# Kernel tuning notes

Measured on AMD Instinct MI355X. Metric: run time of the kernel, lower is better.

The kernel has to match this reference:

```python
import jax, jax.numpy as jnp
import numpy as np

DIM = 1024; HEADS = 8; DHEAD = 64; INNER = HEADS * DHEAD
WS = 512; B = 2; N = 2048; FF = 4 * DIM
NEG = -1e9


def layernorm(x, g, b, eps=1e-5):
    mu = jnp.mean(x, -1, keepdims=True)
    var = jnp.mean((x - mu) ** 2, -1, keepdims=True)
    return (x - mu) * jax.lax.rsqrt(var + eps) * g + b


def rmsnorm(x, g, eps=1e-6):
    return x * jax.lax.rsqrt(jnp.mean(x * x, -1, keepdims=True) + eps) * g


def rotate_half(x):
    x1, x2 = jnp.split(x, 2, -1)
    return jnp.concatenate([-x2, x1], -1)


def local_attention(q, k, v):
    # lucidrains LocalAttention: single-head over last dim, rotary pos emb,
    # window_size=WS, causal, look_backward=1, look_forward=0. n % WS == 0 so autopad no-op.
    b, n, d = q.shape
    w = n // WS
    inv_freq = 1.0 / (10000.0 ** (jnp.arange(0, d, 2, dtype=jnp.float32) / d))
    t = jnp.arange(n)
    freqs = t[:, None].astype(jnp.float32) * inv_freq[None, :]
    emb = jnp.concatenate([freqs, freqs], -1)           # [n, d]
    cos, sin = jnp.cos(emb), jnp.sin(emb)
    q = q * cos + rotate_half(q) * sin
    k = k * cos + rotate_half(k) * sin
    bq = q.reshape(b, w, WS, d) * (d ** -0.5)
    bk = k.reshape(b, w, WS, d)
    bv = v.reshape(b, w, WS, d)

    def look_around(x, pad_value):
        # gather current window + 1 window backward along the window axis
        pads = [(0, 0), (1, 0)] + [(0, 0)] * (x.ndim - 2)
        xp = jnp.pad(x, pads, constant_values=pad_value)
        return jnp.concatenate([xp[:, 0:w], xp[:, 1:w + 1]], axis=2)

    bk = look_around(bk, 0.0)                 # [b, w, 2*WS, d]
    bv = look_around(bv, 0.0)
    bt = t.reshape(w, WS)                     # query positions per window
    bqk = look_around(bt[None], -1)[0]        # key positions, pad = -1  [w, 2*WS]
    sim = jnp.einsum('bwie,bwje->bwij', bq, bk)  # [b, w, WS, 2*WS]
    mask = (bt[:, :, None] < bqk[:, None, :]) | (bqk[:, None, :] == -1)
    sim = jnp.where(mask[None], NEG, sim)
    attn = jax.nn.softmax(sim, -1)
    out = jnp.einsum('bwij,bwje->bwie', attn, bv)
    return out.reshape(b, n, d)


def setup_inputs() -> dict:
    key = jax.random.key(0)
    ks = jax.random.split(key, 10)
    s = 0.02
    f32 = jnp.float32
    return {
        'text': jax.random.normal(ks[0], (B, N, DIM), f32),
        'audio': jax.random.normal(ks[1], (B, N, DIM), f32),
        'video': jax.random.normal(ks[2], (B, N, DIM), f32),
        'Wa': jax.random.normal(ks[3], (DIM, DIM), f32) * s,
        'ba': jnp.zeros((DIM,), f32),
        'lna_g': jnp.ones((DIM,), f32), 'lna_b': jnp.zeros((DIM,), f32),
        'Wvid': jax.random.normal(ks[4], (DIM, DIM), f32) * s,
        'bvid': jnp.zeros((DIM,), f32),
        'lnv_g': jnp.ones((DIM,), f32), 'lnv_b': jnp.zeros((DIM,), f32),
        'ln1_g': jnp.ones((DIM,), f32), 'ln1_b': jnp.zeros((DIM,), f32),
        'Wq': jax.random.normal(ks[5], (DIM, INNER), f32) * s,
        'Wkv': jax.random.normal(ks[6], (DIM, 2 * INNER), f32) * s,
        'qn_g': jnp.ones((DHEAD,), f32), 'kn_g': jnp.ones((DHEAD,), f32),
        'Wo': jax.random.normal(ks[7], (INNER, DIM), f32) * s,
        'W1': jax.random.normal(ks[8], (DIM, FF), f32) * s,
        'b1': jnp.zeros((FF,), f32),
        'ln2_g': jnp.ones((FF,), f32), 'ln2_b': jnp.zeros((FF,), f32),
        'W2': jax.random.normal(ks[9], (FF, DIM), f32) * s,
        'b2': jnp.zeros((DIM,), f32),
    }


def reference(text, audio, video, Wa, ba, lna_g, lna_b, Wvid, bvid, lnv_g, lnv_b,
              ln1_g, ln1_b, Wq, Wkv, qn_g, kn_g, Wo, W1, b1, ln2_g, ln2_b, W2, b2):
    # modality -> text-token adapters (audio_to_text / video_to_text): linear + layernorm
    audio_t = layernorm(audio @ Wa + ba, lna_g, lna_b)
    video_t = layernorm(video @ Wvid + bvid, lnv_g, lnv_b)
    # windowed local attention: q=text, k=audio tokens, v=video tokens
    x = local_attention(text, audio_t, video_t)          # [B, N, DIM]
    # qk-norm full causal attention (flash=False: dense [B,H,N,N] scores)
    b, n, _ = x.shape
    h = layernorm(x, ln1_g, ln1_b)
    q = (h @ Wq).reshape(b, n, HEADS, DHEAD).transpose(0, 2, 1, 3)
    k, v = jnp.split(h @ Wkv, 2, -1)
    k = k.reshape(b, n, HEADS, DHEAD).transpose(0, 2, 1, 3)
    v = v.reshape(b, n, HEADS, DHEAD).transpose(0, 2, 1, 3)
    q = rmsnorm(q, qn_g)
    k = rmsnorm(k, kn_g)
    sim = jnp.einsum('bhid,bhjd->bhij', q, k) * (DHEAD ** -0.5)
    causal = jnp.tril(jnp.ones((n, n), bool))
    sim = jnp.where(causal[None, None], sim, NEG)
    attn = jax.nn.softmax(sim, -1)
    o = jnp.einsum('bhij,bhjd->bhid', attn, v).transpose(0, 2, 1, 3).reshape(b, n, INNER)
    x = o @ Wo
    x = x + x                                            # x = x + x in source
    # FFN: Linear -> GELU -> post-act LayerNorm -> Linear, + residual
    h1 = layernorm(jax.nn.gelu(x @ W1 + b1), ln2_g, ln2_b)
    return h1 @ W2 + b2 + x
```

## Files before the change

kernel.cpp:

```cpp
#include <hip/hip_runtime.h>
#include <hip/hip_bf16.h>

typedef __bf16 bf16;
typedef __bf16 bf16x8 __attribute__((ext_vector_type(8)));
typedef float  f32x4  __attribute__((ext_vector_type(4)));

static __device__ __forceinline__ float b2f(bf16 x) { return (float)x; }
static __device__ __forceinline__ bf16  f2b(float x) { return (bf16)x; }
static __device__ __forceinline__ float ldval(float v) { return v; }
static __device__ __forceinline__ float ldval(bf16 v)  { return (float)v; }

static __device__ __forceinline__ void gl_lds16(const bf16* g, bf16* l)
{
    __builtin_amdgcn_global_load_lds(
        (const __attribute__((address_space(1))) void*)g,
        (__attribute__((address_space(3))) void*)l,
        16, 0, 0);
}

__global__ void detect_dtype(const unsigned short* __restrict__ p, int* __restrict__ flag)
{
    if (threadIdx.x == 0 && blockIdx.x == 0) {
        int big = 0;
        for (int i = 0; i < 512; ++i) {
            int e = (p[i] >> 7) & 0xFF;
            if (e >= 0xE0) big++;
        }
        *flag = (big > 0) ? 1 : 0;
    }
}

__global__ __launch_bounds__(256) void convert2(
    const void* __restrict__ sa, const void* __restrict__ sb,
    bf16* __restrict__ da, bf16* __restrict__ db, int n,
    const int* __restrict__ flag)
{
    int f = *flag;
    int half = gridDim.x >> 1;
    const void* s = (blockIdx.x < half) ? sa : sb;
    bf16* d = (blockIdx.x < half) ? da : db;
    int bid = (blockIdx.x < half) ? blockIdx.x : blockIdx.x - half;
    for (int i = bid * 256 + threadIdx.x; i < n; i += half * 256) {
        float v = f ? ((const float*)s)[i] : (float)((const bf16*)s)[i];
        d[i] = f2b(v);
    }
}

struct VecPack { const void* src[14]; int n[14]; };
__global__ __launch_bounds__(256) void convert_vecs(
    VecPack vp, bf16* __restrict__ dst, const int* __restrict__ flag)
{
    int v = blockIdx.x;
    int f = *flag;
    const void* s = vp.src[v];
    int n = vp.n[v];
    bf16* d = dst + (size_t)v * 4096;
    for (int i = threadIdx.x; i < n; i += 256) {
        float x = f ? ((const float*)s)[i] : (float)((const bf16*)s)[i];
        d[i] = f2b(x);
    }
}

template <int EPI, int MT>
__global__ __launch_bounds__(256) void gemm_bt(
    const bf16* __restrict__ A0, int lda, int zsA, int zsA2,
    const bf16* __restrict__ B0, int ldb, int zsB, int zsB2,
    void* __restrict__ C0, int ldc, int zsC, int zsC2,
    const bf16* __restrict__ bias, int zsBias, float scale, int K)
{
    constexpr int IFR = MT / 32;
    __shared__ __align__(16) bf16 As[MT * 64];
    __shared__ __align__(16) bf16 Bs[128 * 64];
    const int z = blockIdx.z;
    const bf16* A  = A0 + (size_t)z * zsA + (size_t)(z >> 2) * zsA2;
    const bf16* Bt = B0 + (size_t)z * zsB + (size_t)(z >> 2) * zsB2;
    const size_t cbase = (size_t)z * zsC + (size_t)(z >> 2) * zsC2;
    if (bias) bias += (size_t)z * zsBias;
    const int tid  = threadIdx.x;
    const int lane = tid & 63, wave = tid >> 6;
    const int quad = lane >> 4, l16 = lane & 15;
    const size_t tm = (size_t)blockIdx.y * MT, tn = (size_t)blockIdx.x * 128;
    const int wm = (wave >> 1) * (MT / 2), wn = (wave & 1) * 64;
    const int srow = lane >> 3;
    const int scol = ((lane & 7) ^ srow) * 8;

    f32x4 acc[IFR][4];
    const f32x4 zro = {0.f, 0.f, 0.f, 0.f};
    #pragma unroll
    for (int i = 0; i < IFR; ++i)
        #pragma unroll
        for (int j = 0; j < 4; ++j) acc[i][j] = zro;

    const int swzA = l16 & 7;
    for (int k0 = 0; k0 < K; k0 += 64) {
        #pragma unroll
        for (int i = 0; i < IFR; ++i) {
            int chunk = (wave * IFR + i) * 64;
            int row = (chunk >> 3) + srow;
            gl_lds16(A + (tm + row) * (size_t)lda + k0 + scol, As + (size_t)chunk * 8);
        }
        #pragma unroll
        for (int i = 0; i < 4; ++i) {
            int chunk = (wave * 4 + i) * 64;
            int row = (chunk >> 3) + srow;
            gl_lds16(Bt + (tn + row) * (size_t)ldb + k0 + scol, Bs + (size_t)chunk * 8);
        }
        __syncthreads();
        #pragma unroll
        for (int kk = 0; kk < 2; ++kk) {
            bf16x8 af[IFR], bfr[4];
            #pragma unroll
            for (int i = 0; i < IFR; ++i) {
                int row = wm + i * 16 + l16;
                af[i] = *(const bf16x8*)(const void*)&As[(row * 8 + ((kk*4 + quad) ^ swzA)) * 8];
            }
            #pragma unroll
            for (int j = 0; j < 4; ++j) {
                int row = wn + j * 16 + l16;
                bfr[j] = *(const bf16x8*)(const void*)&Bs[(row * 8 + ((kk*4 + quad) ^ swzA)) * 8];
            }
            #pragma unroll
            for (int i = 0; i < IFR; ++i)
                #pragma unroll
                for (int j = 0; j < 4; ++j)
                    acc[i][j] = __builtin_amdgcn_mfma_f32_16x16x32_bf16(
                        af[i], bfr[j], acc[i][j], 0, 0, 0);
        }
        __syncthreads();
    }

    float* Cf = (float*)C0;
    bf16*  Cb = (bf16*)C0;
    #pragma unroll
    for (int i = 0; i < IFR; ++i) {
        #pragma unroll
        for (int j = 0; j < 4; ++j) {
            size_t col = tn + wn + j*16 + l16;
            float bb = bias ? b2f(bias[col]) : 0.f;
            #pragma unroll
            for (int r = 0; r < 4; ++r) {
                size_t row = tm + wm + i*16 + quad*4 + r;
                float v = acc[i][j][r] + bb;
                size_t off = cbase + row * (size_t)ldc + col;
                if (EPI == 0) {
                    Cf[off] = v;
                } else if (EPI == 1) {
                    Cb[off] = f2b(v * scale);
                } else {
                    float g = 0.5f * v * (1.f + tanhf(0.7978845608028654f *
                                  (v + 0.044715f * v * v * v)));
                    Cb[off] = f2b(g);
                }
            }
        }
    }
}

__global__ __launch_bounds__(512, 2) void gemm_ff1_8ph(
    const bf16* __restrict__ A, int lda,
    const bf16* __restrict__ Bt, int ldb,
    bf16* __restrict__ C, int ldc,
    const bf16* __restrict__ bias, int K)
{
    __shared__ __align__(16) bf16 As[2][256 * 64];
    __shared__ __align__(16) bf16 Bs[2][256 * 64];
    const int tid  = threadIdx.x;
    const int lane = tid & 63, wave = tid >> 6;
    const int quad = lane >> 4, l16 = lane & 15;
    const int wr = wave >> 2, wc = wave & 3;
    const size_t tm = (size_t)blockIdx.y * 256;
    const size_t tn = (size_t)blockIdx.x * 256;
    const int srow = lane >> 3;
    const int scol = ((lane & 7) ^ srow) * 8;
    const int swz  = l16 & 7;

    f32x4 acc[8][4];
    const f32x4 zro = {0.f, 0.f, 0.f, 0.f};
    #pragma unroll
    for (int m = 0; m < 8; ++m)
        #pragma unroll
        for (int n = 0; n < 4; ++n) acc[m][n] = zro;

    const bf16* aSrc[4];
    const bf16* bSrc[4];
    #pragma unroll
    for (int i = 0; i < 4; ++i) {
        int grow = wave * 32 + i * 8 + srow;
        aSrc[i] = A  + (tm + grow) * (size_t)lda + scol;
        bSrc[i] = Bt + (tn + grow) * (size_t)ldb + scol;
    }

#define STAGE(BUF, K0, I)                                                     \
    do {                                                                      \
        gl_lds16(aSrc[I] + (K0), &As[BUF][(wave * 4 + (I)) * 512]);           \
        gl_lds16(bSrc[I] + (K0), &Bs[BUF][(wave * 4 + (I)) * 512]);           \
    } while (0)

#define LDA_F(BUF, M, KK)                                                     \
    (*(const bf16x8*)(const void*)&As[BUF][(wr * 128 + (M) * 16 + l16) * 64 + \
        ((((KK) * 4 + quad) ^ swz) << 3)])
#define LDB_F(BUF, N, KK)                                                     \
    (*(const bf16x8*)(const void*)&Bs[BUF][(wc * 64 + (N) * 16 + l16) * 64 +  \
        ((((KK) * 4 + quad) ^ swz) << 3)])

#define PHASE(M0, M1, PREF_STMT, TAIL_STMT)                                   \
    {                                                                         \
        PREF_STMT;                                                            \
        bf16x8 x0 = LDA_F(cur, M0, 0), x1 = LDA_F(cur, M0, 1);                \
        bf16x8 y0 = LDA_F(cur, M1, 0), y1 = LDA_F(cur, M1, 1);                \
        asm volatile("s_barrier" ::: "memory");                               \
        __builtin_amdgcn_s_setprio(1);                                        \
        _Pragma("unroll")                                                     \
        for (int n = 0; n < 4; ++n) {                                         \
            acc[M0][n] = __builtin_amdgcn_mfma_f32_16x16x32_bf16(x0, bfr[n][0], acc[M0][n], 0, 0, 0); \
            acc[M0][n] = __builtin_amdgcn_mfma_f32_16x16x32_bf16(x1, bfr[n][1], acc[M0][n], 0, 0, 0); \
            acc[M1][n] = __builtin_amdgcn_mfma_f32_16x16x32_bf16(y0, bfr[n][0], acc[M1][n], 0, 0, 0); \
            acc[M1][n] = __builtin_amdgcn_mfma_f32_16x16x32_bf16(y1, bfr[n][1], acc[M1][n], 0, 0, 0); \
        }                                                                     \
        __builtin_amdgcn_s_setprio(0);                                        \
        TAIL_STMT;                                                            \
        asm volatile("s_barrier" ::: "memory");                               \
    }

    #pragma unroll
    for (int i = 0; i < 4; ++i) STAGE(0, 0, i);
    asm volatile("s_waitcnt vmcnt(0)" ::: "memory");
    asm volatile("s_barrier" ::: "memory");

    const int NT = K >> 6;
    bf16x8 bfr[4][2];
    for (int t = 0; t < NT; ++t) {
        const int cur = t & 1, nxt = cur ^ 1;
        const int k1  = (t + 1) << 6;
        const bool pref = (t + 1 < NT);

        #pragma unroll
        for (int n = 0; n < 4; ++n) {
            bfr[n][0] = LDB_F(cur, n, 0);
            bfr[n][1] = LDB_F(cur, n, 1);
        }
        PHASE(0, 1,
              if (pref) { STAGE(nxt, k1, 0); STAGE(nxt, k1, 1); }, )
        PHASE(2, 3,
              if (pref) { STAGE(nxt, k1, 2); STAGE(nxt, k1, 3); }, )
        PHASE(4, 5, , )
        PHASE(6, 7, ,
              asm volatile("s_waitcnt vmcnt(0)" ::: "memory"))
    }
#undef PHASE
#undef LDB_F
#undef LDA_F
#undef STAGE

    #pragma unroll
    for (int m = 0; m < 8; ++m) {
        #pragma unroll
        for (int n = 0; n < 4; ++n) {
            size_t col = tn + wc * 64 + n * 16 + l16;
            float bb = b2f(bias[col]);
            #pragma unroll
            for (int r = 0; r < 4; ++r) {
                size_t row = tm + wr * 128 + m * 16 + quad * 4 + r;
                float v = acc[m][n][r] + bb;
                float s = v * (1.5957691216057308f + 0.07135481627f * v * v);
                float g = v / (1.f + __expf(-s));
                C[row * (size_t)ldc + col] = f2b(g);
            }
        }
    }
}

__global__ void transpose_any(const void* __restrict__ in, int R, int C,
                              unsigned short* __restrict__ out, int ldo,
                              const int* __restrict__ flag)
{
    __shared__ unsigned short t[32][33];
    int f = *flag;
    int c0 = blockIdx.x * 32, r0 = blockIdx.y * 32;
    int tx = threadIdx.x, ty = threadIdx.y;
    for (int i = ty; i < 32; i += 8) {
        size_t idx = (size_t)(r0 + i) * C + c0 + tx;
        bf16 v = f ? f2b(((const float*)in)[idx]) : ((const bf16*)in)[idx];
        t[i][tx] = *(unsigned short*)&v;
    }
    __syncthreads();
    for (int i = ty; i < 32; i += 8)
        out[(size_t)(c0 + i) * ldo + r0 + tx] = t[tx][i];
}

__global__ void transpose_vt(const unsigned short* __restrict__ in,
                             unsigned short* __restrict__ out)
{
    __shared__ unsigned short t[32][33];
    int b = blockIdx.z;
    const unsigned short* src = in + (size_t)b * 2048 * 1024;
    unsigned short* dst = out + (size_t)b * 1024 * 2560;
    int c0 = blockIdx.x * 32, r0 = blockIdx.y * 32;
    int tx = threadIdx.x, ty = threadIdx.y;
    for (int i = ty; i < 32; i += 8)
        t[i][tx] = src[(size_t)(r0 + i) * 1024 + c0 + tx];
    __syncthreads();
    for (int i = ty; i < 32; i += 8)
        dst[(size_t)(c0 + i) * 2560 + 512 + r0 + tx] = t[tx][i];
}

__global__ void transpose_v(const float* __restrict__ qkv, bf16* __restrict__ Vt)
{
    __shared__ float t[32][33];
    int bh = blockIdx.z, b = bh >> 3, h = bh & 7;
    const float* src = qkv + (size_t)b * 2048 * 1536 + 1024 + h * 64;
    int c0 = blockIdx.x * 32, r0 = blockIdx.y * 32;
    int tx = threadIdx.x, ty = threadIdx.y;
    for (int i = ty; i < 32; i += 8)
        t[i][tx] = src[(size_t)(r0 + i) * 1536 + c0 + tx];
    __syncthreads();
    bf16* dst = Vt + (size_t)bh * 64 * 2048;
    for (int i = ty; i < 32; i += 8)
        dst[(size_t)(c0 + i) * 2048 + r0 + tx] = f2b(t[tx][i]);
}

template <typename Tin>
__global__ __launch_bounds__(256) void ln_rows(
    const Tin* __restrict__ in, int C,
    const bf16* __restrict__ g, const bf16* __restrict__ b,
    bf16* __restrict__ out, float eps)
{
    const int row = blockIdx.x, tid = threadIdx.x;
    const Tin* p = in + (size_t)row * C;
    float s = 0.f, ss = 0.f;
    for (int c = tid; c < C; c += 256) {
        float v = ldval(p[c]);
        s += v; ss += v * v;
    }
    #pragma unroll
    for (int d = 32; d > 0; d >>= 1) { s += __shfl_xor(s, d); ss += __shfl_xor(ss, d); }
    __shared__ float red[2][4];
    int wave = tid >> 6, lane = tid & 63;
    if (lane == 0) { red[0][wave] = s; red[1][wave] = ss; }
    __syncthreads();
    s  = red[0][0] + red[0][1] + red[0][2] + red[0][3];
    ss = red[1][0] + red[1][1] + red[1][2] + red[1][3];
    float mu   = s / C;
    float var  = ss / C - mu * mu;
    float rstd = rsqrtf(var + eps);
    bf16* q = out + (size_t)row * C;
    for (int c = tid; c < C; c += 256) {
        float v = ldval(p[c]);
        q[c] = f2b((v - mu) * rstd * b2f(g[c]) + b2f(b[c]));
    }
}

__global__ __launch_bounds__(256) void ln_rows2(
    const bf16* __restrict__ in,
    const bf16* __restrict__ g0, const bf16* __restrict__ b0,
    const bf16* __restrict__ g1, const bf16* __restrict__ b1,
    bf16* __restrict__ out0, bf16* __restrict__ out1)
{
    const int row = blockIdx.x, tid = threadIdx.x;
    const int sel = row >> 12;
    const bf16* p = in + (size_t)row * 1024;
    const bf16* g = sel ? g1 : g0;
    const bf16* b = sel ? b1 : b0;
    bf16* q = (sel ? out1 + (size_t)(row - 4096) * 1024 : out0 + (size_t)row * 1024);
    float s = 0.f, ss = 0.f;
    for (int c = tid; c < 1024; c += 256) {
        float v = b2f(p[c]);
        s += v; ss += v * v;
    }
    #pragma unroll
    for (int d = 32; d > 0; d >>= 1) { s += __shfl_xor(s, d); ss += __shfl_xor(ss, d); }
    __shared__ float red[2][4];
    int wave = tid >> 6, lane = tid & 63;
    if (lane == 0) { red[0][wave] = s; red[1][wave] = ss; }
    __syncthreads();
    s  = red[0][0] + red[0][1] + red[0][2] + red[0][3];
    ss = red[1][0] + red[1][1] + red[1][2] + red[1][3];
    float mu   = s * (1.f / 1024.f);
    float var  = ss * (1.f / 1024.f) - mu * mu;
    float rstd = rsqrtf(var + 1e-5f);
    for (int c = tid; c < 1024; c += 256) {
        float v = b2f(p[c]);
        q[c] = f2b((v - mu) * rstd * b2f(g[c]) + b2f(b[c]));
    }
}

__global__ __launch_bounds__(256) void rotary_kernel(
    const void* __restrict__ text, const int* __restrict__ flag,
    const bf16* __restrict__ audioT,
    bf16* __restrict__ qrot, bf16* __restrict__ krotPad)
{
    int row = blockIdx.x;
    int t = row & 2047, b = row >> 11;
    int tid = threadIdx.x;
    int f = *flag;
    const float lg = 9.210340371976184f / 512.f;
    size_t base = (size_t)row * 1024;
    size_t kb = ((size_t)(b * 2560 + 512 + t)) * 1024;
    for (int c = tid; c < 512; c += 256) {
        float invf = __expf(-(float)c * lg);
        float th = (float)t * invf;
        float sn, cs;
        sincosf(th, &sn, &cs);
        float q1 = f ? ((const float*)text)[base + c]
                     : b2f(((const bf16*)text)[base + c]);
        float q2 = f ? ((const float*)text)[base + c + 512]
                     : b2f(((const bf16*)text)[base + c + 512]);
        qrot[base + c]       = f2b((q1 * cs - q2 * sn) * 0.03125f);
        qrot[base + c + 512] = f2b((q2 * cs + q1 * sn) * 0.03125f);
        float k1 = b2f(audioT[base + c]), k2 = b2f(audioT[base + c + 512]);
        krotPad[kb + c]       = f2b(k1 * cs - k2 * sn);
        krotPad[kb + c + 512] = f2b(k2 * cs + k1 * sn);
    }
}

__global__ __launch_bounds__(256) void softmax_local(
    const float* __restrict__ sim, bf16* __restrict__ attn)
{
    int i  = blockIdx.x;
    int zz = blockIdx.y;
    int w  = zz & 3;
    int tid = threadIdx.x;
    const float* p = sim + ((size_t)zz * 512 + i) * 1024;
    bf16* q = attn + ((size_t)zz * 512 + i) * 1024;
    int jlo = (w == 0) ? 512 : 0;
    int jhi = 512 + i;
    float m = -1e30f;
    #pragma unroll
    for (int k = 0; k < 4; ++k) {
        int c = tid + k * 256;
        if (c >= jlo && c <= jhi) m = fmaxf(m, p[c]);
    }
    #pragma unroll
    for (int d = 32; d > 0; d >>= 1) m = fmaxf(m, __shfl_xor(m, d));
    __shared__ float red[2][4];
    int wave = tid >> 6, lane = tid & 63;
    if (lane == 0) red[0][wave] = m;
    __syncthreads();
    m = fmaxf(fmaxf(red[0][0], red[0][1]), fmaxf(red[0][2], red[0][3]));
    float pv[4];
    float s = 0.f;
    #pragma unroll
    for (int k = 0; k < 4; ++k) {
        int c = tid + k * 256;
        float e = (c >= jlo && c <= jhi) ? __expf(p[c] - m) : 0.f;
        pv[k] = e; s += e;
    }
    #pragma unroll
    for (int d = 32; d > 0; d >>= 1) s += __shfl_xor(s, d);
    if (lane == 0) red[1][wave] = s;
    __syncthreads();
    s = red[1][0] + red[1][1] + red[1][2] + red[1][3];
    float inv = 1.f / s;
    #pragma unroll
    for (int k = 0; k < 4; ++k) q[tid + k * 256] = f2b(pv[k] * inv);
}

__global__ __launch_bounds__(256) void pack_qk(
    const float* __restrict__ qkv, bf16* __restrict__ Qp, bf16* __restrict__ Kp,
    const bf16* __restrict__ qn_g, const bf16* __restrict__ kn_g)
{
    int gid  = blockIdx.x * 4 + (threadIdx.x >> 6);
    int lane = threadIdx.x & 63;
    int token = gid >> 4, r = gid & 15, part = r >> 3, h = r & 7;
    const float* p = qkv + (size_t)token * 1536 + part * 512 + h * 64 + lane;
    float v = *p;
    float ss = v * v;
    #pragma unroll
    for (int d = 32; d > 0; d >>= 1) ss += __shfl_xor(ss, d);
    float sc = rsqrtf(ss * (1.f / 64.f) + 1e-6f);
    const bf16* gw = part ? kn_g : qn_g;
    float outv = v * sc * b2f(gw[lane]);
    if (!part) outv *= 0.125f;
    int b = token >> 11, t = token & 2047;
    bf16* dst = (part ? Kp : Qp) + ((size_t)(b * 8 + h) * 2048 + t) * 64 + lane;
    *dst = f2b(outv);
}

__global__ __launch_bounds__(256) void flash_fused(
    const bf16* __restrict__ Qp, const bf16* __restrict__ Kp,
    const bf16* __restrict__ Vt, bf16* __restrict__ o)
{
    __shared__ __align__(16) bf16 Ks[2][64][72];
    __shared__ __align__(16) bf16 Vs[2][64][72];
    __shared__ __align__(16) bf16 Ps[4][16][72];
    const int qb = 31 - blockIdx.x;
    const int bh = blockIdx.y, b = bh >> 3, h = bh & 7;
    const int qm = qb * 64;
    const int tid = threadIdx.x, wave = tid >> 6, lane = tid & 63;
    const int quad = lane >> 4, l16 = lane & 15;
    const bf16* Qg = Qp + (size_t)bh * 2048 * 64;
    const bf16* Kg = Kp + (size_t)bh * 2048 * 64;
    const bf16* Vg = Vt + (size_t)bh * 64 * 2048;

    const int qrow = qm + wave * 16 + l16;
    bf16x8 qa[2];
    qa[0] = *(const bf16x8*)(const void*)(Qg + (size_t)qrow * 64 + quad * 8);
    qa[1] = *(const bf16x8*)(const void*)(Qg + (size_t)qrow * 64 + 32 + quad * 8);

    f32x4 oacc[4];
    const f32x4 zro = {0.f, 0.f, 0.f, 0.f};
    #pragma unroll
    for (int j = 0; j < 4; ++j) oacc[j] = zro;
    float mst[4] = {-1e30f, -1e30f, -1e30f, -1e30f};
    float lst[4] = {0.f, 0.f, 0.f, 0.f};

    const int ldr = tid >> 2, ldc = (tid & 3) * 16;
    {
        uint4 ka = *(const uint4*)(const void*)(Kg + (size_t)ldr * 64 + ldc);
        uint4 kb = *(const uint4*)(const void*)(Kg + (size_t)ldr * 64 + ldc + 8);
        uint4 va = *(const uint4*)(const void*)(Vg + (size_t)ldr * 2048 + ldc);
        uint4 vb = *(const uint4*)(const void*)(Vg + (size_t)ldr * 2048 + ldc + 8);
        *(uint4*)(void*)&Ks[0][ldr][ldc]     = ka;
        *(uint4*)(void*)&Ks[0][ldr][ldc + 8] = kb;
        *(uint4*)(void*)&Vs[0][ldr][ldc]     = va;
        *(uint4*)(void*)&Vs[0][ldr][ldc + 8] = vb;
    }
    __syncthreads();

    const int ntiles = qb + 1;
    for (int t = 0; t < ntiles; ++t) {
        const int cur = t & 1, nxt = cur ^ 1;
        const int jt = t * 64;
        const bool pref = (t + 1 < ntiles);
        uint4 ka, kb, va, vb;
        if (pref) {
            int jn = jt + 64;
            ka = *(const uint4*)(const void*)(Kg + (size_t)(jn + ldr) * 64 + ldc);
            kb = *(const uint4*)(const void*)(Kg + (size_t)(jn + ldr) * 64 + ldc + 8);
            va = *(const uint4*)(const void*)(Vg + (size_t)ldr * 2048 + jn + ldc);
            vb = *(const uint4*)(const void*)(Vg + (size_t)ldr * 2048 + jn + ldc + 8);
        }

        f32x4 s[4];
        #pragma unroll
        for (int j = 0; j < 4; ++j) s[j] = zro;
        #pragma unroll
        for (int kk = 0; kk < 2; ++kk) {
            #pragma unroll
            for (int j = 0; j < 4; ++j) {
                bf16x8 kf = *(const bf16x8*)(const void*)&Ks[cur][j*16 + l16][kk*32 + quad*8];
                s[j] = __builtin_amdgcn_mfma_f32_16x16x32_bf16(qa[kk], kf, s[j], 0, 0, 0);
            }
        }

        if (jt + 63 > qm + wave * 16) {
            #pragma unroll
            for (int j = 0; j < 4; ++j) {
                int key = jt + j * 16 + l16;
                #pragma unroll
                for (int r = 0; r < 4; ++r) {
                    int row = qm + wave * 16 + quad * 4 + r;
                    if (key > row) s[j][r] = -1e30f;
                }
            }
        }

        f32x4 tmax = s[0];
        #pragma unroll
        for (int j = 1; j < 4; ++j)
            #pragma unroll
            for (int r = 0; r < 4; ++r) tmax[r] = fmaxf(tmax[r], s[j][r]);
        #pragma unroll
        for (int r = 0; r < 4; ++r) {
            float tv = tmax[r];
            #pragma unroll
            for (int d = 1; d < 16; d <<= 1) tv = fmaxf(tv, __shfl_xor(tv, d));
            tmax[r] = tv;
        }
        float scl[4];
        #pragma unroll
        for (int r = 0; r < 4; ++r) {
            float mn = fmaxf(mst[r], tmax[r]);
            scl[r] = __expf(mst[r] - mn);
            mst[r] = mn;
        }
        f32x4 psum = zro;
        #pragma unroll
        for (int j = 0; j < 4; ++j)
            #pragma unroll
            for (int r = 0; r < 4; ++r) {
                float e = __expf(s[j][r] - mst[r]);
                s[j][r] = e;
                psum[r] += e;
            }
        #pragma unroll
        for (int r = 0; r < 4; ++r) {
            float tv = psum[r];
            #pragma unroll
            for (int d = 1; d < 16; d <<= 1) tv += __shfl_xor(tv, d);
            lst[r] = lst[r] * scl[r] + tv;
        }
        #pragma unroll
        for (int j = 0; j < 4; ++j)
            #pragma unroll
            for (int r = 0; r < 4; ++r) oacc[j][r] *= scl[r];

        #pragma unroll
        for (int j = 0; j < 4; ++j)
            #pragma unroll
            for (int r = 0; r < 4; ++r)
                Ps[wave][quad*4 + r][j*16 + l16] = f2b(s[j][r]);
        bf16x8 pa[2];
        pa[0] = *(const bf16x8*)(const void*)&Ps[wave][l16][quad*8];
        pa[1] = *(const bf16x8*)(const void*)&Ps[wave][l16][32 + quad*8];

        #pragma unroll
        for (int kk = 0; kk < 2; ++kk) {
            #pragma unroll
            for (int j = 0; j < 4; ++j) {
                bf16x8 vf = *(const bf16x8*)(const void*)&Vs[cur][j*16 + l16][kk*32 + quad*8];
                oacc[j] = __builtin_amdgcn_mfma_f32_16x16x32_bf16(pa[kk], vf, oacc[j], 0, 0, 0);
            }
        }

        if (pref) {
            *(uint4*)(void*)&Ks[nxt][ldr][ldc]     = ka;
            *(uint4*)(void*)&Ks[nxt][ldr][ldc + 8] = kb;
            *(uint4*)(void*)&Vs[nxt][ldr][ldc]     = va;
            *(uint4*)(void*)&Vs[nxt][ldr][ldc + 8] = vb;
            __syncthreads();
        }
    }

    #pragma unroll
    for (int j = 0; j < 4; ++j) {
        #pragma unroll
        for (int r = 0; r < 4; ++r) {
            int t = qm + wave * 16 + quad * 4 + r;
            o[((size_t)(b * 2048 + t)) * 512 + h * 64 + j * 16 + l16] =
                f2b(oacc[j][r] / lst[r]);
        }
    }
}

__global__ __launch_bounds__(256) void combine_ff2(
    const float* __restrict__ p0, const float* __restrict__ p1,
    const bf16* __restrict__ x2, const bf16* __restrict__ b2,
    float* __restrict__ out)
{
    int i4 = (blockIdx.x * 256 + threadIdx.x) * 4;
    #pragma unroll
    for (int k = 0; k < 4; ++k) {
        int i = i4 + k;
        out[i] = p0[i] + p1[i] + b2f(x2[i]) + b2f(b2[i & 1023]);
    }
}

static void launch_gemm(int epi, hipStream_t s,
                        const bf16* A, int lda, int zsA, int zsA2,
                        const bf16* Bt, int ldb, int zsB, int zsB2,
                        void* C, int ldc, int zsC, int zsC2,
                        const bf16* bias, int zsBias, float scale,
                        int M, int N, int K, int nz)
{
    bool mt64 = ((M >> 7) * (N >> 7) * nz) <= 512;
    dim3 blk(256);
    if (mt64) {
        dim3 g(N / 128, M / 64, nz);
        switch (epi) {
        case 0: gemm_bt<0,64><<<g, blk, 0, s>>>(A, lda, zsA, zsA2, Bt, ldb, zsB, zsB2, C, ldc, zsC, zsC2, bias, zsBias, scale, K); break;
        case 1: gemm_bt<1,64><<<g, blk, 0, s>>>(A, lda, zsA, zsA2, Bt, ldb, zsB, zsB2, C, ldc, zsC, zsC2, bias, zsBias, scale, K); break;
        default: gemm_bt<2,64><<<g, blk, 0, s>>>(A, lda, zsA, zsA2, Bt, ldb, zsB, zsB2, C, ldc, zsC, zsC2, bias, zsBias, scale, K); break;
        }
    } else {
        dim3 g(N / 128, M / 128, nz);
        switch (epi) {
        case 0: gemm_bt<0,128><<<g, blk, 0, s>>>(A, lda, zsA, zsA2, Bt, ldb, zsB, zsB2, C, ldc, zsC, zsC2, bias, zsBias, scale, K); break;
        case 1: gemm_bt<1,128><<<g, blk, 0, s>>>(A, lda, zsA, zsA2, Bt, ldb, zsB, zsB2, C, ldc, zsC, zsC2, bias, zsBias, scale, K); break;
        default: gemm_bt<2,128><<<g, blk, 0, s>>>(A, lda, zsA, zsA2, Bt, ldb, zsB, zsB2, C, ldc, zsC, zsC2, bias, zsBias, scale, K); break;
        }
    }
}

extern "C" void kernel_launch(void* const* d_in, const int* in_sizes, int n_in,
                              void* d_out, int out_size, void* d_ws, size_t ws_size,
                              hipStream_t stream)
{
    const void* text  = d_in[0];
    const void* audio = d_in[1];
    const void* video = d_in[2];
    const void* Wa    = d_in[3];
    const void* ba    = d_in[4];
    const void* lna_g = d_in[5];
    const void* lna_b = d_in[6];
    const void* Wvid  = d_in[7];
    const void* bvid  = d_in[8];
    const void* lnv_g = d_in[9];
    const void* lnv_b = d_in[10];
    const void* ln1_g = d_in[11];
    const void* ln1_b = d_in[12];
    const void* Wq    = d_in[13];
    const void* Wkv   = d_in[14];
    const void* qn_g  = d_in[15];
    const void* kn_g  = d_in[16];
    const void* Wo    = d_in[17];
    const void* W1    = d_in[18];
    const void* b1    = d_in[19];
    const void* ln2_g = d_in[20];
    const void* ln2_b = d_in[21];
    const void* W2    = d_in[22];
    const void* b2    = d_in[23];

    char* ws = (char*)d_ws;
    size_t off = 0;
    auto alloc = [&](size_t bytes) -> char* {
        char* p = ws + off;
        off += (bytes + 255) & ~(size_t)255;
        return p;
    };
    const size_t MB = 1024 * 1024;
    int*  flag  = (int*)alloc(256);
    bf16* vecs  = (bf16*)alloc(14 * 4096 * 2);
    bf16* WqkvT = (bf16*)alloc((size_t)1536 * 1024 * 2);
    bf16* WoT   = (bf16*)alloc((size_t)1024 * 512 * 2);
    bf16* W1T   = (bf16*)alloc((size_t)4096 * 1024 * 2);
    bf16* W2T   = (bf16*)alloc((size_t)1024 * 4096 * 2);
    char* regionIn = alloc(24 * MB);
    char* region2  = alloc(32 * MB);
    char* regionH  = alloc(8 * MB);
    char* regionX  = alloc(8 * MB);
    char* regionO  = alloc(4 * MB);
    bf16* qrot    = (bf16*)alloc((size_t)4096 * 1024 * 2);
    bf16* krotPad = (bf16*)alloc((size_t)2 * 2560 * 1024 * 2);
    bf16* VTpad   = (bf16*)alloc((size_t)2 * 1024 * 2560 * 2);
    bf16* attn    = (bf16*)alloc((size_t)8 * 512 * 1024 * 2);

    bf16*  audioC = (bf16*)regionIn;
    bf16*  videoC = audioC + (size_t)4096 * 1024;
    float* qkvF   = (float*)regionIn;
    bf16*  tmp2   = (bf16*)region2;
    float* tmpF   = (float*)region2;
    float* xF     = (float*)(region2 + 16 * MB);
    bf16*  g      = (bf16*)region2;
    bf16*  audioT = (bf16*)regionH;
    bf16*  h      = (bf16*)regionH;
    bf16*  videoT = (bf16*)regionX;
    bf16*  x2     = (bf16*)regionX;
    bf16*  WaT    = (bf16*)regionO;
    bf16*  WvT    = WaT + (size_t)1024 * 1024;
    bf16*  o      = (bf16*)regionO;
    bf16*  Qp     = qrot;
    bf16*  Kp     = krotPad;
    bf16*  Vth    = attn;
    float* p0     = (float*)regionIn;
    float* p1     = (float*)VTpad;

    bf16* baC   = vecs + 0 * 4096;
    bf16* bvidC = vecs + 1 * 4096;
    bf16* lnagC = vecs + 2 * 4096;
    bf16* lnabC = vecs + 3 * 4096;
    bf16* lnvgC = vecs + 4 * 4096;
    bf16* lnvbC = vecs + 5 * 4096;
    bf16* ln1gC = vecs + 6 * 4096;
    bf16* ln1bC = vecs + 7 * 4096;
    bf16* qngC  = vecs + 8 * 4096;
    bf16* kngC  = vecs + 9 * 4096;
    bf16* b1C   = vecs + 10 * 4096;
    bf16* ln2gC = vecs + 11 * 4096;
    bf16* ln2bC = vecs + 12 * 4096;
    bf16* b2C   = vecs + 13 * 4096;

    detect_dtype<<<1, 64, 0, stream>>>((const unsigned short*)text, flag);

    const int NTOK = 4096 * 1024;
    convert2<<<4096, 256, 0, stream>>>(audio, video, audioC, videoC, NTOK, flag);
    VecPack vp;
    const void* vsrc[14] = {ba, bvid, lna_g, lna_b, lnv_g, lnv_b, ln1_g, ln1_b,
                            qn_g, kn_g, b1, ln2_g, ln2_b, b2};
    int vn[14] = {1024, 1024, 1024, 1024, 1024, 1024, 1024, 1024,
                  64, 64, 4096, 4096, 4096, 1024};
    for (int i = 0; i < 14; ++i) { vp.src[i] = vsrc[i]; vp.n[i] = vn[i]; }
    convert_vecs<<<14, 256, 0, stream>>>(vp, vecs, flag);

    dim3 tb(32, 8);
    transpose_any<<<dim3(32, 32), tb, 0, stream>>>(Wa, 1024, 1024, (unsigned short*)WaT, 1024, flag);
    transpose_any<<<dim3(32, 32), tb, 0, stream>>>(Wvid, 1024, 1024, (unsigned short*)WvT, 1024, flag);
    transpose_any<<<dim3(16, 32), tb, 0, stream>>>(Wq, 1024, 512, (unsigned short*)WqkvT, 1024, flag);
    transpose_any<<<dim3(32, 32), tb, 0, stream>>>(Wkv, 1024, 1024, (unsigned short*)(WqkvT + (size_t)512 * 1024), 1024, flag);
    transpose_any<<<dim3(32, 16), tb, 0, stream>>>(Wo, 512, 1024, (unsigned short*)WoT, 512, flag);
    transpose_any<<<dim3(128, 32), tb, 0, stream>>>(W1, 1024, 4096, (unsigned short*)W1T, 1024, flag);
    transpose_any<<<dim3(32, 128), tb, 0, stream>>>(W2, 4096, 1024, (unsigned short*)W2T, 4096, flag);

    launch_gemm(1, stream, audioC, 1024, 4096*1024, 0, WaT, 1024, 1024*1024, 0,
                tmp2, 1024, 4096*1024, 0, baC, 4096, 1.f, 4096, 1024, 1024, 2);
    ln_rows2<<<8192, 256, 0, stream>>>(tmp2, lnagC, lnabC, lnvgC, lnvbC, audioT, videoT);

    hipMemsetAsync(krotPad, 0, (size_t)2 * 2560 * 1024 * 2, stream);
    hipMemsetAsync(VTpad, 0, (size_t)2 * 1024 * 2560 * 2, stream);
    rotary_kernel<<<4096, 256, 0, stream>>>(text, flag, audioT, qrot, krotPad);
    transpose_vt<<<dim3(32, 64, 2), tb, 0, stream>>>(
        (const unsigned short*)videoT, (unsigned short*)VTpad);

    launch_gemm(0, stream, qrot, 1024, 512*1024, 0,
                krotPad, 1024, 512*1024, 512*1024,
                tmpF, 1024, 512*1024, 0, nullptr, 0, 1.f, 512, 1024, 1024, 8);
    softmax_local<<<dim3(512, 8), 256, 0, stream>>>(tmpF, attn);
    launch_gemm(0, stream, attn, 1024, 512*1024, 0,
                VTpad, 2560, 512, 1024*2560 - 2048,
                xF, 1024, 512*1024, 0, nullptr, 0, 1.f, 512, 1024, 1024, 8);

    ln_rows<float><<<4096, 256, 0, stream>>>(xF, 1024, ln1gC, ln1bC, h, 1e-5f);
    launch_gemm(0, stream, h, 1024, 0, 0, WqkvT, 1024, 0, 0,
                qkvF, 1536, 0, 0, nullptr, 0, 1.f, 4096, 1536, 1024, 1);
    pack_qk<<<16384, 256, 0, stream>>>(qkvF, Qp, Kp, qngC, kngC);
    transpose_v<<<dim3(2, 64, 16), tb, 0, stream>>>(qkvF, Vth);
    flash_fused<<<dim3(32, 16), 256, 0, stream>>>(Qp, Kp, Vth, o);

    launch_gemm(1, stream, o, 512, 0, 0, WoT, 512, 0, 0,
                x2, 1024, 0, 0, nullptr, 0, 2.f, 4096, 1024, 512, 1);
    gemm_ff1_8ph<<<dim3(16, 16), 512, 0, stream>>>(x2, 1024, W1T, 1024,
                                                   g, 4096, b1C, 1024);
    ln_rows<bf16><<<4096, 256, 0, stream>>>(g, 4096, ln2gC, ln2bC, g, 1e-5f);
    launch_gemm(0, stream, g, 4096, 2048, 0, W2T, 4096, 2048, 0,
                p0, 1024, (int)(p1 - p0), 0, nullptr, 0, 1.f, 4096, 1024, 2048, 2);
    combine_ff2<<<4096, 256, 0, stream>>>(p0, p1, x2, b2C, (float*)d_out);

    (void)in_sizes; (void)n_in; (void)out_size; (void)ws_size;
}
```

Baseline: 578.6 us.

## Rewrite causal flash attention to load K/V straight into registers per wave

The flash attention kernel becomes 128-thread blocks of two independent 16-row query waves. Each wave loads K and V fragments from global memory directly into registers, double-buffered in a register ping-pong, and the shared-memory K/V tiles and block barriers are removed. The S matrix is computed transposed (K as the A operand), so the row max and sum need only two cross-lane shuffles, and causal work is balanced at 16-row granularity. In exchange, each wave re-reads K/V from global or L2 memory with no sharing across waves, and register pressure rises.

```diff
diff --git a/kernel.cpp b/kernel.cpp
--- a/kernel.cpp
+++ b/kernel.cpp
@@ -476,159 +476,141 @@
     *dst = f2b(outv);
 }
 
-__global__ __launch_bounds__(256) void flash_fused(
+__global__ __launch_bounds__(128, 2) void flash_fused2(
     const bf16* __restrict__ Qp, const bf16* __restrict__ Kp,
     const bf16* __restrict__ Vt, bf16* __restrict__ o)
 {
-    __shared__ __align__(16) bf16 Ks[2][64][72];
-    __shared__ __align__(16) bf16 Vs[2][64][72];
-    __shared__ __align__(16) bf16 Ps[4][16][72];
-    const int qb = 31 - blockIdx.x;
+    __shared__ __align__(16) bf16 Ps[2][16][72];
+    const int wav  = threadIdx.x >> 6;
+    const int lane = threadIdx.x & 63;
+    const int quad = lane >> 4, l16 = lane & 15;
+    const int qrow16 = (63 - blockIdx.x) * 2 + wav;
     const int bh = blockIdx.y, b = bh >> 3, h = bh & 7;
-    const int qm = qb * 64;
-    const int tid = threadIdx.x, wave = tid >> 6, lane = tid & 63;
-    const int quad = lane >> 4, l16 = lane & 15;
+    const int qm = qrow16 * 16;
     const bf16* Qg = Qp + (size_t)bh * 2048 * 64;
     const bf16* Kg = Kp + (size_t)bh * 2048 * 64;
     const bf16* Vg = Vt + (size_t)bh * 64 * 2048;
 
-    const int qrow = qm + wave * 16 + l16;
     bf16x8 qa[2];
-    qa[0] = *(const bf16x8*)(const void*)(Qg + (size_t)qrow * 64 + quad * 8);
-    qa[1] = *(const bf16x8*)(const void*)(Qg + (size_t)qrow * 64 + 32 + quad * 8);
-
+    qa[0] = *(const bf16x8*)(const void*)(Qg + (size_t)(qm + l16) * 64 + quad * 8);
+    qa[1] = *(const bf16x8*)(const void*)(Qg + (size_t)(qm + l16) * 64 + 32 + quad * 8);
+
+    const f32x4 zro = {0.f, 0.f, 0.f, 0.f};
     f32x4 oacc[4];
-    const f32x4 zro = {0.f, 0.f, 0.f, 0.f};
     #pragma unroll
     for (int j = 0; j < 4; ++j) oacc[j] = zro;
-    float mst[4] = {-1e30f, -1e30f, -1e30f, -1e30f};
-    float lst[4] = {0.f, 0.f, 0.f, 0.f};
-
-    const int ldr = tid >> 2, ldc = (tid & 3) * 16;
-    {
-        uint4 ka = *(const uint4*)(const void*)(Kg + (size_t)ldr * 64 + ldc);
-        uint4 kb = *(const uint4*)(const void*)(Kg + (size_t)ldr * 64 + ldc + 8);
-        uint4 va = *(const uint4*)(const void*)(Vg + (size_t)ldr * 2048 + ldc);
-        uint4 vb = *(const uint4*)(const void*)(Vg + (size_t)ldr * 2048 + ldc + 8);
-        *(uint4*)(void*)&Ks[0][ldr][ldc]     = ka;
-        *(uint4*)(void*)&Ks[0][ldr][ldc + 8] = kb;
-        *(uint4*)(void*)&Vs[0][ldr][ldc]     = va;
-        *(uint4*)(void*)&Vs[0][ldr][ldc + 8] = vb;
-    }
-    __syncthreads();
-
-    const int ntiles = qb + 1;
-    for (int t = 0; t < ntiles; ++t) {
-        const int cur = t & 1, nxt = cur ^ 1;
-        const int jt = t * 64;
-        const bool pref = (t + 1 < ntiles);
-        uint4 ka, kb, va, vb;
-        if (pref) {
-            int jn = jt + 64;
-            ka = *(const uint4*)(const void*)(Kg + (size_t)(jn + ldr) * 64 + ldc);
-            kb = *(const uint4*)(const void*)(Kg + (size_t)(jn + ldr) * 64 + ldc + 8);
-            va = *(const uint4*)(const void*)(Vg + (size_t)ldr * 2048 + jn + ldc);
-            vb = *(const uint4*)(const void*)(Vg + (size_t)ldr * 2048 + jn + ldc + 8);
-        }
-
-        f32x4 s[4];
-        #pragma unroll
-        for (int j = 0; j < 4; ++j) s[j] = zro;
-        #pragma unroll
-        for (int kk = 0; kk < 2; ++kk) {
-            #pragma unroll
-            for (int j = 0; j < 4; ++j) {
-                bf16x8 kf = *(const bf16x8*)(const void*)&Ks[cur][j*16 + l16][kk*32 + quad*8];
-                s[j] = __builtin_amdgcn_mfma_f32_16x16x32_bf16(qa[kk], kf, s[j], 0, 0, 0);
-            }
-        }
-
-        if (jt + 63 > qm + wave * 16) {
-            #pragma unroll
-            for (int j = 0; j < 4; ++j) {
-                int key = jt + j * 16 + l16;
-                #pragma unroll
-                for (int r = 0; r < 4; ++r) {
-                    int row = qm + wave * 16 + quad * 4 + r;
-                    if (key > row) s[j][r] = -1e30f;
-                }
-            }
-        }
-
-        f32x4 tmax = s[0];
-        #pragma unroll
-        for (int j = 1; j < 4; ++j)
-            #pragma unroll
-            for (int r = 0; r < 4; ++r) tmax[r] = fmaxf(tmax[r], s[j][r]);
-        #pragma unroll
-        for (int r = 0; r < 4; ++r) {
-            float tv = tmax[r];
-            #pragma unroll
-            for (int d = 1; d < 16; d <<= 1) tv = fmaxf(tv, __shfl_xor(tv, d));
-            tmax[r] = tv;
-        }
-        float scl[4];
-        #pragma unroll
-        for (int r = 0; r < 4; ++r) {
-            float mn = fmaxf(mst[r], tmax[r]);
-            scl[r] = __expf(mst[r] - mn);
-            mst[r] = mn;
-        }
-        f32x4 psum = zro;
-        #pragma unroll
-        for (int j = 0; j < 4; ++j)
-            #pragma unroll
-            for (int r = 0; r < 4; ++r) {
-                float e = __expf(s[j][r] - mst[r]);
-                s[j][r] = e;
-                psum[r] += e;
-            }
-        #pragma unroll
-        for (int r = 0; r < 4; ++r) {
-            float tv = psum[r];
-            #pragma unroll
-            for (int d = 1; d < 16; d <<= 1) tv += __shfl_xor(tv, d);
-            lst[r] = lst[r] * scl[r] + tv;
-        }
-        #pragma unroll
-        for (int j = 0; j < 4; ++j)
-            #pragma unroll
-            for (int r = 0; r < 4; ++r) oacc[j][r] *= scl[r];
-
-        #pragma unroll
-        for (int j = 0; j < 4; ++j)
-            #pragma unroll
-            for (int r = 0; r < 4; ++r)
-                Ps[wave][quad*4 + r][j*16 + l16] = f2b(s[j][r]);
-        bf16x8 pa[2];
-        pa[0] = *(const bf16x8*)(const void*)&Ps[wave][l16][quad*8];
-        pa[1] = *(const bf16x8*)(const void*)&Ps[wave][l16][32 + quad*8];
-
-        #pragma unroll
-        for (int kk = 0; kk < 2; ++kk) {
-            #pragma unroll
-            for (int j = 0; j < 4; ++j) {
-                bf16x8 vf = *(const bf16x8*)(const void*)&Vs[cur][j*16 + l16][kk*32 + quad*8];
-                oacc[j] = __builtin_amdgcn_mfma_f32_16x16x32_bf16(pa[kk], vf, oacc[j], 0, 0, 0);
-            }
-        }
-
-        if (pref) {
-            *(uint4*)(void*)&Ks[nxt][ldr][ldc]     = ka;
-            *(uint4*)(void*)&Ks[nxt][ldr][ldc + 8] = kb;
-            *(uint4*)(void*)&Vs[nxt][ldr][ldc]     = va;
-            *(uint4*)(void*)&Vs[nxt][ldr][ldc + 8] = vb;
-            __syncthreads();
-        }
-    }
-
+    float mst = -1e30f, lst = 0.f;
+    const int q_row = qm + l16;
+    const int nt = (qrow16 >> 2) + 1;
+
+#define LOADSET(KF, VF, T)                                                    \
+    {                                                                         \
+        const int jt_ = (T) * 64;                                             \
+        _Pragma("unroll")                                                     \
+        for (int j = 0; j < 4; ++j) {                                         \
+            KF[j][0] = *(const bf16x8*)(const void*)(Kg +                     \
+                (size_t)(jt_ + j*16 + l16) * 64 + quad * 8);                  \
+            KF[j][1] = *(const bf16x8*)(const void*)(Kg +                     \
+                (size_t)(jt_ + j*16 + l16) * 64 + 32 + quad * 8);             \
+            VF[j][0] = *(const bf16x8*)(const void*)(Vg +                     \
+                (size_t)(j*16 + l16) * 2048 + jt_ + quad * 8);                \
+            VF[j][1] = *(const bf16x8*)(const void*)(Vg +                     \
+                (size_t)(j*16 + l16) * 2048 + jt_ + 32 + quad * 8);           \
+        }                                                                     \
+    }
+
+#define COMPUTE(KF, VF, T)                                                    \
+    {                                                                         \
+        const int jt_ = (T) * 64;                                             \
+        f32x4 s[4];                                                           \
+        _Pragma("unroll")                                                     \
+        for (int j = 0; j < 4; ++j) s[j] = zro;                               \
+        _Pragma("unroll")                                                     \
+        for (int kk = 0; kk < 2; ++kk)                                        \
+            _Pragma("unroll")                                                 \
+            for (int j = 0; j < 4; ++j)                                       \
+                s[j] = __builtin_amdgcn_mfma_f32_16x16x32_bf16(               \
+                    KF[j][kk], qa[kk], s[j], 0, 0, 0);                        \
+        if (jt_ + 63 > qm) {                                                  \
+            _Pragma("unroll")                                                 \
+            for (int j = 0; j < 4; ++j)                                       \
+                _Pragma("unroll")                                             \
+                for (int r = 0; r < 4; ++r) {                                 \
+                    int key = jt_ + j * 16 + quad * 4 + r;                    \
+                    if (key > q_row) s[j][r] = -1e30f;                        \
+                }                                                             \
+        }                                                                     \
+        float m16 = -1e30f;                                                   \
+        _Pragma("unroll")                                                     \
+        for (int j = 0; j < 4; ++j)                                           \
+            _Pragma("unroll")                                                 \
+            for (int r = 0; r < 4; ++r) m16 = fmaxf(m16, s[j][r]);            \
+        m16 = fmaxf(m16, __shfl_xor(m16, 16));                                \
+        m16 = fmaxf(m16, __shfl_xor(m16, 32));                                \
+        float mn  = fmaxf(mst, m16);                                          \
+        float scl = __expf(mst - mn);                                         \
+        mst = mn;                                                             \
+        float ts = 0.f;                                                       \
+        _Pragma("unroll")                                                     \
+        for (int j = 0; j < 4; ++j)                                           \
+            _Pragma("unroll")                                                 \
+            for (int r = 0; r < 4; ++r) {                                     \
+                float e = __expf(s[j][r] - mn);                               \
+                s[j][r] = e; ts += e;                                         \
+            }                                                                 \
+        ts += __shfl_xor(ts, 16);                                             \
+        ts += __shfl_xor(ts, 32);                                             \
+        lst = lst * scl + ts;                                                 \
+        float sclq[4];                                                        \
+        _Pragma("unroll")                                                     \
+        for (int r = 0; r < 4; ++r) sclq[r] = __shfl(scl, quad * 4 + r);      \
+        _Pragma("unroll")                                                     \
+        for (int j = 0; j < 4; ++j)                                           \
+            _Pragma("unroll")                                                 \
+            for (int r = 0; r < 4; ++r) oacc[j][r] *= sclq[r];                \
+        _Pragma("unroll")                                                     \
+        for (int j = 0; j < 4; ++j) {                                         \
+            union { bf16 hx[4]; uint2 u; } pk;                                \
+            pk.hx[0] = f2b(s[j][0]); pk.hx[1] = f2b(s[j][1]);                 \
+            pk.hx[2] = f2b(s[j][2]); pk.hx[3] = f2b(s[j][3]);                 \
+            *(uint2*)(void*)&Ps[wav][l16][j * 16 + quad * 4] = pk.u;          \
+        }                                                                     \
+        bf16x8 pf0 = *(const bf16x8*)(const void*)&Ps[wav][l16][quad * 8];    \
+        bf16x8 pf1 = *(const bf16x8*)(const void*)&Ps[wav][l16][32 + quad*8]; \
+        _Pragma("unroll")                                                     \
+        for (int j = 0; j < 4; ++j)                                           \
+            oacc[j] = __builtin_amdgcn_mfma_f32_16x16x32_bf16(                \
+                pf0, VF[j][0], oacc[j], 0, 0, 0);                             \
+        _Pragma("unroll")                                                     \
+        for (int j = 0; j < 4; ++j)                                           \
+            oacc[j] = __builtin_amdgcn_mfma_f32_16x16x32_bf16(                \
+                pf1, VF[j][1], oacc[j], 0, 0, 0);                             \
+    }
+
+    bf16x8 kA[4][2], vA[4][2], kB[4][2], vB[4][2];
+    LOADSET(kA, vA, 0);
+    int t = 0;
+    for (;;) {
+        if (t + 1 < nt) LOADSET(kB, vB, t + 1);
+        COMPUTE(kA, vA, t);
+        ++t; if (t >= nt) break;
+        if (t + 1 < nt) LOADSET(kA, vA, t + 1);
+        COMPUTE(kB, vB, t);
+        ++t; if (t >= nt) break;
+    }
+#undef COMPUTE
+#undef LOADSET
+
+    float invq[4];
+    #pragma unroll
+    for (int r = 0; r < 4; ++r) invq[r] = 1.f / __shfl(lst, quad * 4 + r);
     #pragma unroll
     for (int j = 0; j < 4; ++j) {
         #pragma unroll
         for (int r = 0; r < 4; ++r) {
-            int t = qm + wave * 16 + quad * 4 + r;
-            o[((size_t)(b * 2048 + t)) * 512 + h * 64 + j * 16 + l16] =
-                f2b(oacc[j][r] / lst[r]);
+            int tr = qm + quad * 4 + r;
+            o[((size_t)(b * 2048 + tr)) * 512 + h * 64 + j * 16 + l16] =
+                f2b(oacc[j][r] * invq[r]);
         }
     }
 }
@@ -804,7 +786,7 @@
                 qkvF, 1536, 0, 0, nullptr, 0, 1.f, 4096, 1536, 1024, 1);
     pack_qk<<<16384, 256, 0, stream>>>(qkvF, Qp, Kp, qngC, kngC);
     transpose_v<<<dim3(2, 64, 16), tb, 0, stream>>>(qkvF, Vth);
-    flash_fused<<<dim3(32, 16), 256, 0, stream>>>(Qp, Kp, Vth, o);
+    flash_fused2<<<dim3(64, 16), 128, 0, stream>>>(Qp, Kp, Vth, o);
 
     launch_gemm(1, stream, o, 512, 0, 0, WoT, 512, 0, 0,
                 x2, 1024, 0, 0, nullptr, 0, 2.f, 4096, 1024, 512, 1);
```

New measurement: 630.5 us. +9.0%, slower.

## Shrink flash attention blocks to 32 query rows with single-buffered KV tiles

Applied to the files above, without the earlier changes.

Replaces the 256-thread flash attention kernel, which handled 64 query rows with double-buffered K/V tiles, by a 128-thread variant covering 32 query rows with a single K/V buffer. Block count doubles to 1024 and the launch bounds request three blocks per SM, aiming for finer causal load balance and higher occupancy on the triangular workload. In exchange the register prefetch of the next tile is dropped, so global loads are no longer overlapped with MFMA work. K/V tiles are also loaded twice as often overall, since each block now covers half as many query rows.

```diff
diff --git a/kernel.cpp b/kernel.cpp
--- a/kernel.cpp
+++ b/kernel.cpp
@@ -476,16 +476,16 @@
     *dst = f2b(outv);
 }
 
-__global__ __launch_bounds__(256) void flash_fused(
+__global__ __launch_bounds__(128, 3) void flash_fused3(
     const bf16* __restrict__ Qp, const bf16* __restrict__ Kp,
     const bf16* __restrict__ Vt, bf16* __restrict__ o)
 {
-    __shared__ __align__(16) bf16 Ks[2][64][72];
-    __shared__ __align__(16) bf16 Vs[2][64][72];
-    __shared__ __align__(16) bf16 Ps[4][16][72];
-    const int qb = 31 - blockIdx.x;
+    __shared__ __align__(16) bf16 Ks[64][72];
+    __shared__ __align__(16) bf16 Vs[64][72];
+    __shared__ __align__(16) bf16 Ps[2][16][72];
+    const int qb = 63 - blockIdx.x;
     const int bh = blockIdx.y, b = bh >> 3, h = bh & 7;
-    const int qm = qb * 64;
+    const int qm = qb * 32;
     const int tid = threadIdx.x, wave = tid >> 6, lane = tid & 63;
     const int quad = lane >> 4, l16 = lane & 15;
     const bf16* Qg = Qp + (size_t)bh * 2048 * 64;
@@ -504,32 +504,18 @@
     float mst[4] = {-1e30f, -1e30f, -1e30f, -1e30f};
     float lst[4] = {0.f, 0.f, 0.f, 0.f};
 
-    const int ldr = tid >> 2, ldc = (tid & 3) * 16;
-    {
-        uint4 ka = *(const uint4*)(const void*)(Kg + (size_t)ldr * 64 + ldc);
-        uint4 kb = *(const uint4*)(const void*)(Kg + (size_t)ldr * 64 + ldc + 8);
-        uint4 va = *(const uint4*)(const void*)(Vg + (size_t)ldr * 2048 + ldc);
-        uint4 vb = *(const uint4*)(const void*)(Vg + (size_t)ldr * 2048 + ldc + 8);
-        *(uint4*)(void*)&Ks[0][ldr][ldc]     = ka;
-        *(uint4*)(void*)&Ks[0][ldr][ldc + 8] = kb;
-        *(uint4*)(void*)&Vs[0][ldr][ldc]     = va;
-        *(uint4*)(void*)&Vs[0][ldr][ldc + 8] = vb;
-    }
-    __syncthreads();
-
-    const int ntiles = qb + 1;
+    const int ldr = tid >> 1, ldc = (tid & 1) * 32;
+    const int ntiles = (qb >> 1) + 1;
     for (int t = 0; t < ntiles; ++t) {
-        const int cur = t & 1, nxt = cur ^ 1;
         const int jt = t * 64;
-        const bool pref = (t + 1 < ntiles);
-        uint4 ka, kb, va, vb;
-        if (pref) {
-            int jn = jt + 64;
-            ka = *(const uint4*)(const void*)(Kg + (size_t)(jn + ldr) * 64 + ldc);
-            kb = *(const uint4*)(const void*)(Kg + (size_t)(jn + ldr) * 64 + ldc + 8);
-            va = *(const uint4*)(const void*)(Vg + (size_t)ldr * 2048 + jn + ldc);
-            vb = *(const uint4*)(const void*)(Vg + (size_t)ldr * 2048 + jn + ldc + 8);
-        }
+        #pragma unroll
+        for (int c = 0; c < 4; ++c) {
+            *(uint4*)(void*)&Ks[ldr][ldc + c * 8] =
+                *(const uint4*)(const void*)(Kg + (size_t)(jt + ldr) * 64 + ldc + c * 8);
+            *(uint4*)(void*)&Vs[ldr][ldc + c * 8] =
+                *(const uint4*)(const void*)(Vg + (size_t)ldr * 2048 + jt + ldc + c * 8);
+        }
+        __syncthreads();
 
         f32x4 s[4];
         #pragma unroll
@@ -538,8 +524,8 @@
         for (int kk = 0; kk < 2; ++kk) {
             #pragma unroll
             for (int j = 0; j < 4; ++j) {
-                bf16x8 kf = *(const bf16x8*)(const void*)&Ks[cur][j*16 + l16][kk*32 + quad*8];
-                s[j] = __builtin_amdgcn_mfma_f32_16x16x32_bf16(qa[kk], kf, s[j], 0, 0, 0);
+                bf16x8 kb = *(const bf16x8*)(const void*)&Ks[j*16 + l16][kk*32 + quad*8];
+                s[j] = __builtin_amdgcn_mfma_f32_16x16x32_bf16(qa[kk], kb, s[j], 0, 0, 0);
             }
         }
 
@@ -608,18 +594,11 @@
         for (int kk = 0; kk < 2; ++kk) {
             #pragma unroll
             for (int j = 0; j < 4; ++j) {
-                bf16x8 vf = *(const bf16x8*)(const void*)&Vs[cur][j*16 + l16][kk*32 + quad*8];
-                oacc[j] = __builtin_amdgcn_mfma_f32_16x16x32_bf16(pa[kk], vf, oacc[j], 0, 0, 0);
+                bf16x8 vb = *(const bf16x8*)(const void*)&Vs[j*16 + l16][kk*32 + quad*8];
+                oacc[j] = __builtin_amdgcn_mfma_f32_16x16x32_bf16(pa[kk], vb, oacc[j], 0, 0, 0);
             }
         }
-
-        if (pref) {
-            *(uint4*)(void*)&Ks[nxt][ldr][ldc]     = ka;
-            *(uint4*)(void*)&Ks[nxt][ldr][ldc + 8] = kb;
-            *(uint4*)(void*)&Vs[nxt][ldr][ldc]     = va;
-            *(uint4*)(void*)&Vs[nxt][ldr][ldc + 8] = vb;
-            __syncthreads();
-        }
+        __syncthreads();
     }
 
     #pragma unroll
@@ -804,7 +783,7 @@
                 qkvF, 1536, 0, 0, nullptr, 0, 1.f, 4096, 1536, 1024, 1);
     pack_qk<<<16384, 256, 0, stream>>>(qkvF, Qp, Kp, qngC, kngC);
     transpose_v<<<dim3(2, 64, 16), tb, 0, stream>>>(qkvF, Vth);
-    flash_fused<<<dim3(32, 16), 256, 0, stream>>>(Qp, Kp, Vth, o);
+    flash_fused3<<<dim3(64, 16), 128, 0, stream>>>(Qp, Kp, Vth, o);
 
     launch_gemm(1, stream, o, 512, 0, 0, WoT, 512, 0, 0,
                 x2, 1024, 0, 0, nullptr, 0, 2.f, 4096, 1024, 512, 1);
```

Measured after the change: 581.1 us. Within noise of the previous version (+0.4%).
